# Performance work log

Measured on AMD Instinct MI355X. Metric: run time of the kernel, lower is better.

The kernel has to match this reference:

```python
import jax, jax.numpy as jnp
import numpy as np

D = 256
H = 4
HD = D // H


def rotate_half(x):
    xp = x.reshape(x.shape[:-1] + (-1, 2))
    x1, x2 = xp[..., 0], xp[..., 1]
    return jnp.stack((-x2, x1), axis=-1).reshape(x.shape)


def apply_rope(freqs, t):
    # freqs: [2, B, 1, N, HD]; t: [B, H, N, HD]
    return t * freqs[0] + rotate_half(t) * freqs[1]


def layernorm(x, g, b, eps=1e-5):
    m = jnp.mean(x, axis=-1, keepdims=True)
    v = jnp.var(x, axis=-1, keepdims=True)
    return (x - m) * jax.lax.rsqrt(v + eps) * g + b


def ffn(z, W1, b1, g, be, W2, b2):
    h = layernorm(z @ W1 + b1, g, be)
    h = jax.nn.gelu(h, approximate=False)
    return h @ W2 + b2


def heads_split(t):
    B, N, _ = t.shape
    return t.reshape(B, N, H, HD).transpose(0, 2, 1, 3)  # [B,H,N,HD]


def heads_merge(t):
    B, h, N, hd = t.shape
    return t.transpose(0, 2, 1, 3).reshape(B, N, h * hd)


def sdpa(q, k, v):
    s = q.shape[-1] ** (-0.5)
    sim = jnp.einsum('bhid,bhjd->bhij', q, k) * s
    attn = jax.nn.softmax(sim, axis=-1)
    return jnp.einsum('bhij,bhjd->bhid', attn, v)


def self_block(x, enc, Wqkv, bqkv, Wo, bo, W1, b1, g, be, W2, b2):
    B, N, _ = x.shape
    qkv = (x @ Wqkv + bqkv).reshape(B, N, H, HD, 3).transpose(0, 2, 1, 3, 4)
    q, k, v = qkv[..., 0], qkv[..., 1], qkv[..., 2]
    q = apply_rope(enc, q)
    k = apply_rope(enc, k)
    msg = heads_merge(sdpa(q, k, v)) @ Wo + bo
    return x + ffn(jnp.concatenate([x, msg], axis=-1), W1, b1, g, be, W2, b2)


def cross_block(x0, x1, Wqk, bqk, Wv, bv, Wo, bo, W1, b1, g, be, W2, b2):
    qk0 = heads_split(x0 @ Wqk + bqk)
    qk1 = heads_split(x1 @ Wqk + bqk)
    v0 = heads_split(x0 @ Wv + bv)
    v1 = heads_split(x1 @ Wv + bv)
    s = HD ** (-0.5)
    qk0 = qk0 * (s ** 0.5)
    qk1 = qk1 * (s ** 0.5)
    sim = jnp.einsum('bhid,bhjd->bhij', qk0, qk1)
    attn01 = jax.nn.softmax(sim, axis=-1)
    attn10 = jax.nn.softmax(sim.transpose(0, 1, 3, 2), axis=-1)
    m0 = jnp.einsum('bhij,bhjd->bhid', attn01, v1)
    m1 = jnp.einsum('bhij,bhjd->bhid', attn10, v0)
    m0 = heads_merge(m0) @ Wo + bo
    m1 = heads_merge(m1) @ Wo + bo
    x0 = x0 + ffn(jnp.concatenate([x0, m0], axis=-1), W1, b1, g, be, W2, b2)
    x1 = x1 + ffn(jnp.concatenate([x1, m1], axis=-1), W1, b1, g, be, W2, b2)
    return x0, x1


def setup_inputs() -> dict:
    key = jax.random.key(0)
    ks = jax.random.split(key, 24)
    B, N = 4, 2048
    desc0 = jax.random.normal(ks[0], (B, N, D), jnp.float32)
    desc1 = jax.random.normal(ks[1], (B, N, D), jnp.float32)
    encoding0 = jax.random.uniform(ks[2], (2, B, 1, N, HD), jnp.float32)
    encoding1 = jax.random.uniform(ks[3], (2, B, 1, N, HD), jnp.float32)

    def lin(k, fin, fout):
        k1, k2 = jax.random.split(k)
        W = jax.random.normal(k1, (fin, fout), jnp.float32) * (fin ** -0.5)
        b = jax.random.normal(k2, (fout,), jnp.float32) * 0.01
        return W, b

    Wqkv, bqkv = lin(ks[4], D, 3 * D)
    Wo_s, bo_s = lin(ks[5], D, D)
    W1_s, b1_s = lin(ks[6], 2 * D, 2 * D)
    g_s = jnp.ones((2 * D,), jnp.float32)
    be_s = jnp.zeros((2 * D,), jnp.float32)
    W2_s, b2_s = lin(ks[7], 2 * D, D)
    Wqk_c, bqk_c = lin(ks[8], D, D)
    Wv_c, bv_c = lin(ks[9], D, D)
    Wo_c, bo_c = lin(ks[10], D, D)
    W1_c, b1_c = lin(ks[11], 2 * D, 2 * D)
    g_c = jnp.ones((2 * D,), jnp.float32)
    be_c = jnp.zeros((2 * D,), jnp.float32)
    W2_c, b2_c = lin(ks[12], 2 * D, D)
    return dict(desc0=desc0, desc1=desc1, encoding0=encoding0, encoding1=encoding1,
                Wqkv=Wqkv, bqkv=bqkv, Wo_s=Wo_s, bo_s=bo_s,
                W1_s=W1_s, b1_s=b1_s, g_s=g_s, be_s=be_s, W2_s=W2_s, b2_s=b2_s,
                Wqk_c=Wqk_c, bqk_c=bqk_c, Wv_c=Wv_c, bv_c=bv_c, Wo_c=Wo_c, bo_c=bo_c,
                W1_c=W1_c, b1_c=b1_c, g_c=g_c, be_c=be_c, W2_c=W2_c, b2_c=b2_c)


def reference(desc0, desc1, encoding0, encoding1,
              Wqkv, bqkv, Wo_s, bo_s, W1_s, b1_s, g_s, be_s, W2_s, b2_s,
              Wqk_c, bqk_c, Wv_c, bv_c, Wo_c, bo_c, W1_c, b1_c, g_c, be_c, W2_c, b2_c):
    d0 = self_block(desc0, encoding0, Wqkv, bqkv, Wo_s, bo_s, W1_s, b1_s, g_s, be_s, W2_s, b2_s)
    d1 = self_block(desc1, encoding1, Wqkv, bqkv, Wo_s, bo_s, W1_s, b1_s, g_s, be_s, W2_s, b2_s)
    return cross_block(d0, d1, Wqk_c, bqk_c, Wv_c, bv_c, Wo_c, bo_c, W1_c, b1_c, g_c, be_c, W2_c, b2_c)
```

## Files before the change

kernel.cpp:

```cpp
#include <hip/hip_runtime.h>
#include <math.h>

#define BB 4
#define HH 4
#define NN 2048
#define DD 256
#define HDIM 64
#define NTOK 8192
#define NTOK2 16384

typedef __attribute__((ext_vector_type(8))) __bf16 bf16x8;
typedef __attribute__((ext_vector_type(8))) unsigned short ushort8;
typedef __attribute__((ext_vector_type(4))) float floatx4;
typedef __attribute__((ext_vector_type(4))) short short4v;

union U8 { ushort8 u; bf16x8 b; };
union U4 { unsigned int u[2]; unsigned long long l; short4v s; };

#define MFMA16(a, b, c) __builtin_amdgcn_mfma_f32_16x16x16bf16_1k(a, b, c, 0, 0, 0)

__device__ __forceinline__ unsigned short f2bf(float x) {
    unsigned int u = __float_as_uint(x);
    u += 0x7FFF + ((u >> 16) & 1);
    return (unsigned short)(u >> 16);
}
__device__ __forceinline__ float bf2f(unsigned short u) {
    return __uint_as_float(((unsigned int)u) << 16);
}
__device__ __forceinline__ unsigned int pkbf(float a, float b) {
    return ((__float_as_uint(a) + 0x8000u) >> 16) |
           ((__float_as_uint(b) + 0x8000u) & 0xFFFF0000u);
}
__device__ __forceinline__ unsigned int cvtpk(float a, float b) {
    unsigned int r;
    asm("v_cvt_pk_bf16_f32 %0, %1, %2" : "=v"(r) : "v"(a), "v"(b));
    return r;
}
__device__ __forceinline__ floatx4 fmax4(floatx4 a, floatx4 b) {
    floatx4 r;
    r[0] = fmaxf(a[0], b[0]); r[1] = fmaxf(a[1], b[1]);
    r[2] = fmaxf(a[2], b[2]); r[3] = fmaxf(a[3], b[3]);
    return r;
}

struct WTab {
    const float* w[7];
    unsigned short* o[7];
    int K[7];
    int N[7];
    int st[7];
    int t0[8];
};

__global__ __launch_bounds__(256) void wtrans(WTab tab)
{
    __shared__ float lds[32][33];
    const int t = threadIdx.x;
    int bid = blockIdx.x;
    int s = 0;
    while (bid >= tab.t0[s + 1]) s++;
    const int ti = bid - tab.t0[s];
    const int K = tab.K[s], N = tab.N[s], st = tab.st[s];
    const int tx = ti % (N / 32), ty = ti / (N / 32);
    const int k0 = ty * 32, n0 = tx * 32;
    const float* W = tab.w[s];
    unsigned short* Wt = tab.o[s];

    {
        int r = t >> 3, c = (t & 7) * 4;
        float4 a = *(const float4*)&W[(size_t)(k0 + r) * N + n0 + c];
        lds[r][c] = a.x; lds[r][c+1] = a.y; lds[r][c+2] = a.z; lds[r][c+3] = a.w;
    }
    __syncthreads();
    {
        int n = t >> 3, kq = (t & 7) * 4;
        ushort4 p;
        p.x = f2bf(lds[kq+0][n]); p.y = f2bf(lds[kq+1][n]);
        p.z = f2bf(lds[kq+2][n]); p.w = f2bf(lds[kq+3][n]);
        *(ushort4*)&Wt[(size_t)(n0 + n) * st + k0 + kq] = p;
    }
}

__global__ __launch_bounds__(256) void wfuse(
    const float* __restrict__ Wo_s, const float* __restrict__ W1_s,
    unsigned short* __restrict__ o_s,
    const float* __restrict__ Wo_c, const float* __restrict__ W1_c,
    unsigned short* __restrict__ o_c)
{
    __shared__ float wo[32][33];
    __shared__ float w1[32][68];
    const int t = threadIdx.x;
    const int bid = blockIdx.x;
    const int seg = bid >> 6, ti_ = bid & 63;
    const int i0 = (ti_ >> 3) * 32, n0 = (ti_ & 7) * 64;
    const float* Wo  = seg ? Wo_c : Wo_s;
    const float* W1b = (seg ? W1_c : W1_s) + 256 * 512;
    unsigned short* out = seg ? o_c : o_s;
    const int ti = t >> 3, tn = t & 7;

    float acc[8] = {};
    for (int jc = 0; jc < 256; jc += 32) {
        {
            int r = t >> 3, c = (t & 7) * 4;
            *(float4*)&wo[r][c] = *(const float4*)&Wo[(size_t)(i0 + r) * 256 + jc + c];
            int c8 = (t & 7) * 8;
            *(float4*)&w1[r][c8]     = *(const float4*)&W1b[(size_t)(jc + r) * 512 + n0 + c8];
            *(float4*)&w1[r][c8 + 4] = *(const float4*)&W1b[(size_t)(jc + r) * 512 + n0 + c8 + 4];
        }
        __syncthreads();
        #pragma unroll
        for (int j = 0; j < 32; j++) {
            float a = wo[ti][j];
            #pragma unroll
            for (int e = 0; e < 8; e++) acc[e] += a * w1[j][tn * 8 + e];
        }
        __syncthreads();
    }
    #pragma unroll
    for (int e = 0; e < 8; e++)
        out[(size_t)(n0 + tn * 8 + e) * 512 + 256 + i0 + ti] = f2bf(acc[e]);
}

__global__ __launch_bounds__(256) void bfuse(
    const float* bo_s, const float* W1_s, const float* b1_s, float* bs,
    const float* bo_c, const float* W1_c, const float* b1_c, float* bc)
{
    const int seg = blockIdx.x >> 1, half = blockIdx.x & 1;
    const int n = half * 256 + threadIdx.x;
    const float* bo  = seg ? bo_c : bo_s;
    const float* W1b = (seg ? W1_c : W1_s) + 256 * 512;
    const float* b1  = seg ? b1_c : b1_s;
    float* out       = seg ? bc : bs;
    float a = b1[n];
    for (int j = 0; j < 256; j++) a += bo[j] * W1b[(size_t)j * 512 + n];
    out[n] = a;
}

__global__ __launch_bounds__(256) void gemm_mfma(
    const unsigned short* __restrict__ A, int lda,
    const unsigned short* __restrict__ Wt, int K,
    const float* __restrict__ bias, const float* __restrict__ bias2, int mode,
    float* outF, unsigned short* outH0, unsigned short* outH1,
    unsigned short* outH2,
    int ldc, const float* R0, const float* R1)
{
    __shared__ __align__(16) unsigned short As[64 * 40];
    __shared__ __align__(16) unsigned short Bs[128 * 40];
    const int t = threadIdx.x;
    const int w = t >> 6, lane = t & 63, quad = lane >> 4, l15 = lane & 15;
    const int m0 = blockIdx.y * 64, n0 = blockIdx.x * 128;
    const int wn = w * 32;
    const int sar = t >> 2, sac = (t & 3) * 8;
    const int sbr = t >> 1, sbc = (t & 1) * 16;

    const unsigned short* Ap = A  + (size_t)(m0 + sar) * lda + sac;
    const unsigned short* Bp = Wt + (size_t)(n0 + sbr) * K   + sbc;

    ushort8 pa  = *(const ushort8*)(Ap);
    ushort8 pb0 = *(const ushort8*)(Bp);
    ushort8 pb1 = *(const ushort8*)(Bp + 8);

    floatx4 acc[4][2];
    #pragma unroll
    for (int i = 0; i < 4; i++)
        #pragma unroll
        for (int j = 0; j < 2; j++) acc[i][j] = (floatx4){0.f, 0.f, 0.f, 0.f};

    const int nk = K >> 5;
    for (int kk = 0; kk < nk; kk++) {
        *(ushort8*)&As[sar * 40 + sac]     = pa;
        *(ushort8*)&Bs[sbr * 40 + sbc]     = pb0;
        *(ushort8*)&Bs[sbr * 40 + sbc + 8] = pb1;
        __syncthreads();
        if (kk + 1 < nk) {
            int ko = (kk + 1) * 32;
            pa  = *(const ushort8*)(Ap + ko);
            pb0 = *(const ushort8*)(Bp + ko);
            pb1 = *(const ushort8*)(Bp + ko + 8);
        }
        U8 af[4], bf[2];
        #pragma unroll
        for (int i = 0; i < 4; i++)
            af[i].u = *(const ushort8*)&As[(i * 16 + l15) * 40 + quad * 8];
        #pragma unroll
        for (int j = 0; j < 2; j++)
            bf[j].u = *(const ushort8*)&Bs[(wn + j * 16 + l15) * 40 + quad * 8];
        #pragma unroll
        for (int i = 0; i < 4; i++)
            #pragma unroll
            for (int j = 0; j < 2; j++)
                acc[i][j] = __builtin_amdgcn_mfma_f32_16x16x32_bf16(af[i].b, bf[j].b, acc[i][j], 0, 0, 0);
        __syncthreads();
    }

    #pragma unroll
    for (int i = 0; i < 4; i++) {
        #pragma unroll
        for (int j = 0; j < 2; j++) {
            int col = n0 + wn + j * 16 + l15;
            float bv = (mode == 2 && col >= 256) ? bias2[col & 255] : bias[col];
            #pragma unroll
            for (int r = 0; r < 4; r++) {
                int grow = m0 + i * 16 + quad * 4 + r;
                float v = acc[i][j][r] + bv;
                if (mode == 1) {
                    outH0[(size_t)grow * ldc + col] = f2bf(v);
                } else if (mode == 2) {
                    int cc = col & 255;
                    int h = cc >> 6, d = cc & 63;
                    int ds = grow >> 13, b = (grow >> 11) & 3, n = grow & 2047;
                    int bh = ds * 16 + b * 4 + h;
                    if (col < 256)
                        outH0[((size_t)bh * NN + n) * HDIM + d] = f2bf(v);
                    else
                        outH1[((size_t)bh * HDIM + d) * NN + n] = f2bf(v);
                } else if (mode == 3) {
                    int sel = col % 3, cc = col / 3;
                    int h = cc >> 6, d = cc & 63;
                    int ds = grow >> 13, b = (grow >> 11) & 3, n = grow & 2047;
                    int bh = ds * 16 + b * 4 + h;
                    if (sel == 0)
                        outH0[((size_t)bh * NN + n) * HDIM + d] = f2bf(v);
                    else if (sel == 1)
                        outH1[((size_t)bh * NN + n) * HDIM + d] = f2bf(v);
                    else
                        outH2[((size_t)bh * HDIM + d) * NN + n] = f2bf(v);
                } else {
                    const float* R = (grow < NTOK) ? R0 : R1;
                    float vv = v + R[(size_t)(grow & 8191) * 256 + col];
                    outF[(size_t)grow * 256 + col] = vv;
                    if (outH0) outH0[(size_t)grow * 256 + col] = f2bf(vv);
                    if (outH1) outH1[(size_t)grow * 512 + col] = f2bf(vv);
                }
            }
        }
    }
}

__global__ __launch_bounds__(256) void rope_k(unsigned short* __restrict__ qb,
                                              unsigned short* __restrict__ kb,
                                              const float* __restrict__ enc0,
                                              const float* __restrict__ enc1)
{
    int i = blockIdx.x * 256 + threadIdx.x;
    int dp = (i & 31) * 2;
    int n  = (i >> 5) & (NN - 1);
    int h  = (i >> 16) & 3;
    int b  = (i >> 18) & 3;
    int ds = (i >> 20) & 1;
    int bf = (i >> 21) & 1;
    unsigned short* tq = (bf ? kb : qb) +
        (((size_t)(ds * 16 + b * 4 + h)) * NN + n) * HDIM + dp;
    const float* e0 = (ds ? enc1 : enc0) + ((size_t)b * NN + n) * HDIM + dp;
    const float* e1 = e0 + (size_t)BB * NN * HDIM;
    float x0 = bf2f(tq[0]), x1 = bf2f(tq[1]);
    float y0 = x0 * e0[0] - x1 * e1[0];
    float y1 = x1 * e0[1] + x0 * e1[1];
    tq[0] = f2bf(y0); tq[1] = f2bf(y1);
}

__global__ __launch_bounds__(256) void flash_attn(
    const unsigned short* __restrict__ Q, const unsigned short* __restrict__ K,
    const unsigned short* __restrict__ V, unsigned short* __restrict__ O,
    int ldo, int kvx, float qscale)
{
    __shared__ __align__(16) unsigned short Ks[2][64 * 72];
    __shared__ __align__(16) unsigned short Vt[2][64 * 72];

    const int t    = threadIdx.x;
    const int w    = t >> 6;
    const int lane = t & 63;
    const int quad = lane >> 4;
    const int l15  = lane & 15;
    const int bh   = blockIdx.y;
    const int kbh  = bh ^ kvx;
    const int q0   = blockIdx.x * 128;

    const unsigned short* Qb  = Q + (size_t)bh  * NN * HDIM;
    const unsigned short* Kb  = K + (size_t)kbh * NN * HDIM;
    const unsigned short* VTb = V + (size_t)kbh * NN * HDIM;

    const int srf = t >> 3, scf = (t & 7) * 8;

    bf16x8 qf0[2], qf1[2];
    #pragma unroll
    for (int i = 0; i < 2; i++) {
        const int qrow = q0 + w * 32 + i * 16 + l15;
        U8 r0, r1, x0, x1;
        r0.u = *(const ushort8*)&Qb[(size_t)qrow * HDIM + quad * 8];
        r1.u = *(const ushort8*)&Qb[(size_t)qrow * HDIM + 32 + quad * 8];
        #pragma unroll
        for (int j = 0; j < 8; j++) {
            x0.u[j] = f2bf(bf2f(r0.u[j]) * qscale);
            x1.u[j] = f2bf(bf2f(r1.u[j]) * qscale);
        }
        qf0[i] = x0.b; qf1[i] = x1.b;
    }

    floatx4 o[2][4];
    #pragma unroll
    for (int i = 0; i < 2; i++)
        #pragma unroll
        for (int c = 0; c < 4; c++) o[i][c] = (floatx4){0.f, 0.f, 0.f, 0.f};
    float m[2] = {-1e30f, -1e30f};
    float l[2] = {0.f, 0.f};

    ushort8 ka0 = *(const ushort8*)&Kb[(size_t)srf * HDIM + scf];
    ushort8 ka1 = *(const ushort8*)&Kb[(size_t)(srf + 32) * HDIM + scf];
    ushort8 va0 = *(const ushort8*)&VTb[(size_t)srf * NN + scf];
    ushort8 va1 = *(const ushort8*)&VTb[(size_t)(srf + 32) * NN + scf];
    *(ushort8*)&Ks[0][srf * 72 + scf]        = ka0;
    *(ushort8*)&Ks[0][(srf + 32) * 72 + scf] = ka1;
    *(ushort8*)&Vt[0][srf * 72 + scf]        = va0;
    *(ushort8*)&Vt[0][(srf + 32) * 72 + scf] = va1;
    __syncthreads();

    int cur = 0;
    for (int j0 = 0; j0 < NN; j0 += 64, cur ^= 1) {
        const int more = (j0 + 64 < NN);
        if (more) {
            const int jn = j0 + 64;
            ka0 = *(const ushort8*)&Kb[(size_t)(jn + srf) * HDIM + scf];
            ka1 = *(const ushort8*)&Kb[(size_t)(jn + srf + 32) * HDIM + scf];
            va0 = *(const ushort8*)&VTb[(size_t)srf * NN + jn + scf];
            va1 = *(const ushort8*)&VTb[(size_t)(srf + 32) * NN + jn + scf];
        }

        floatx4 s[2][4];
        __builtin_amdgcn_s_setprio(1);
        #pragma unroll
        for (int t4 = 0; t4 < 4; t4++) {
            U8 k0, k1;
            k0.u = *(const ushort8*)&Ks[cur][(t4 * 16 + l15) * 72 + quad * 8];
            k1.u = *(const ushort8*)&Ks[cur][(t4 * 16 + l15) * 72 + 32 + quad * 8];
            #pragma unroll
            for (int i = 0; i < 2; i++) {
                floatx4 z = (floatx4){0.f, 0.f, 0.f, 0.f};
                z = __builtin_amdgcn_mfma_f32_16x16x32_bf16(k0.b, qf0[i], z, 0, 0, 0);
                z = __builtin_amdgcn_mfma_f32_16x16x32_bf16(k1.b, qf1[i], z, 0, 0, 0);
                s[i][t4] = z;
            }
        }
        __builtin_amdgcn_s_setprio(0);

        short4v pf[2][4];
        #pragma unroll
        for (int i = 0; i < 2; i++) {
            floatx4 a = fmax4(fmax4(s[i][0], s[i][1]), fmax4(s[i][2], s[i][3]));
            float mx = fmaxf(fmaxf(a[0], a[1]), fmaxf(a[2], a[3]));
            mx = fmaxf(mx, __shfl_xor(mx, 16, 64));
            mx = fmaxf(mx, __shfl_xor(mx, 32, 64));
            if (!__all(mx <= m[i] + 8.f)) {
                float mn = fmaxf(m[i], mx);
                float al = exp2f(m[i] - mn);
                m[i] = mn;
                l[i] *= al;
                #pragma unroll
                for (int c = 0; c < 4; c++)
                    #pragma unroll
                    for (int r = 0; r < 4; r++) o[i][c][r] *= al;
            }
            float rs = 0.f;
            #pragma unroll
            for (int t4 = 0; t4 < 4; t4++)
                #pragma unroll
                for (int r = 0; r < 4; r++) {
                    float p = exp2f(s[i][t4][r] - m[i]);
                    s[i][t4][r] = p;
                    rs += p;
                }
            rs += __shfl_xor(rs, 16, 64);
            rs += __shfl_xor(rs, 32, 64);
            l[i] += rs;

            #pragma unroll
            for (int t4 = 0; t4 < 4; t4++) {
                U4 pk;
                pk.u[0] = cvtpk(s[i][t4][0], s[i][t4][1]);
                pk.u[1] = cvtpk(s[i][t4][2], s[i][t4][3]);
                pf[i][t4] = pk.s;
            }
        }

        __builtin_amdgcn_s_setprio(1);
        #pragma unroll
        for (int c = 0; c < 4; c++) {
            U4 vf[4];
            #pragma unroll
            for (int t4 = 0; t4 < 4; t4++)
                vf[t4].l = *(const unsigned long long*)
                    &Vt[cur][(c * 16 + l15) * 72 + t4 * 16 + quad * 4];
            #pragma unroll
            for (int i = 0; i < 2; i++)
                #pragma unroll
                for (int t4 = 0; t4 < 4; t4++)
                    o[i][c] = MFMA16(vf[t4].s, pf[i][t4], o[i][c]);
        }
        __builtin_amdgcn_s_setprio(0);

        if (more) {
            *(ushort8*)&Ks[cur ^ 1][srf * 72 + scf]        = ka0;
            *(ushort8*)&Ks[cur ^ 1][(srf + 32) * 72 + scf] = ka1;
            *(ushort8*)&Vt[cur ^ 1][srf * 72 + scf]        = va0;
            *(ushort8*)&Vt[cur ^ 1][(srf + 32) * 72 + scf] = va1;
            __syncthreads();
        }
    }

    const int ds = bh >> 4, b = (bh >> 2) & 3, h = bh & 3;
    #pragma unroll
    for (int i = 0; i < 2; i++) {
        const int q = q0 + w * 32 + i * 16 + l15;
        const size_t row = (size_t)ds * NTOK + b * NN + q;
        float inv = 1.f / l[i];
        #pragma unroll
        for (int c = 0; c < 4; c++) {
            U4 pk;
            pk.u[0] = cvtpk(o[i][c][0] * inv, o[i][c][1] * inv);
            pk.u[1] = cvtpk(o[i][c][2] * inv, o[i][c][3] * inv);
            *(unsigned long long*)&O[row * ldo + h * HDIM + c * 16 + quad * 4] = pk.l;
        }
    }
}

__global__ __launch_bounds__(256) void ln_gelu(
    unsigned short* __restrict__ hb, const float* __restrict__ g,
    const float* __restrict__ be)
{
    __shared__ float r1[4], r2[4];
    const int t = threadIdx.x;
    const size_t row = blockIdx.x;
    unsigned short* ip = hb + row * 512;
    float x0 = bf2f(ip[t]), x1 = bf2f(ip[t + 256]);
    float s = x0 + x1, ss = x0 * x0 + x1 * x1;
    #pragma unroll
    for (int o = 32; o > 0; o >>= 1) { s += __shfl_down(s, o); ss += __shfl_down(ss, o); }
    if ((t & 63) == 0) { r1[t >> 6] = s; r2[t >> 6] = ss; }
    __syncthreads();
    float S  = r1[0] + r1[1] + r1[2] + r1[3];
    float SS = r2[0] + r2[1] + r2[2] + r2[3];
    float mean = S * (1.f / 512.f);
    float var  = SS * (1.f / 512.f) - mean * mean;
    float inv  = rsqrtf(var + 1e-5f);
    float y0 = (x0 - mean) * inv * g[t]       + be[t];
    float y1 = (x1 - mean) * inv * g[t + 256] + be[t + 256];
    ip[t]       = f2bf(0.5f * y0 * (1.f + erff(y0 * 0.70710678f)));
    ip[t + 256] = f2bf(0.5f * y1 * (1.f + erff(y1 * 0.70710678f)));
}

__global__ __launch_bounds__(256) void copy_to_cat(
    const float* __restrict__ s0, const float* __restrict__ s1,
    unsigned short* __restrict__ cat)
{
    int i = blockIdx.x * 256 + threadIdx.x;
    int row = i >> 6, c4 = (i & 63) * 4;
    const float* s = (row < NTOK) ? s0 : s1;
    float4 a = *(const float4*)&s[(size_t)(row & 8191) * 256 + c4];
    ushort4 p = { f2bf(a.x), f2bf(a.y), f2bf(a.z), f2bf(a.w) };
    *(ushort4*)&cat[(size_t)row * 512 + c4] = p;
}

extern "C" void kernel_launch(void* const* d_in, const int* in_sizes, int n_in,
                              void* d_out, int out_size, void* d_ws, size_t ws_size,
                              hipStream_t stream)
{
    const float* desc0 = (const float*)d_in[0];
    const float* desc1 = (const float*)d_in[1];
    const float* enc0  = (const float*)d_in[2];
    const float* enc1  = (const float*)d_in[3];
    const float* Wqkv  = (const float*)d_in[4];  const float* bqkv  = (const float*)d_in[5];
    const float* Wo_s  = (const float*)d_in[6];  const float* bo_s  = (const float*)d_in[7];
    const float* W1_s  = (const float*)d_in[8];  const float* b1_s  = (const float*)d_in[9];
    const float* g_s   = (const float*)d_in[10]; const float* be_s  = (const float*)d_in[11];
    const float* W2_s  = (const float*)d_in[12]; const float* b2_s  = (const float*)d_in[13];
    const float* Wqk_c = (const float*)d_in[14]; const float* bqk_c = (const float*)d_in[15];
    const float* Wv_c  = (const float*)d_in[16]; const float* bv_c  = (const float*)d_in[17];
    const float* Wo_c  = (const float*)d_in[18]; const float* bo_c  = (const float*)d_in[19];
    const float* W1_c  = (const float*)d_in[20]; const float* b1_c  = (const float*)d_in[21];
    const float* g_c   = (const float*)d_in[22]; const float* be_c  = (const float*)d_in[23];
    const float* W2_c  = (const float*)d_in[24]; const float* b2_c  = (const float*)d_in[25];

    char* ws = (char*)d_ws;
    unsigned short* wt  = (unsigned short*)ws;
    unsigned short* qb  = (unsigned short*)(ws + 2490368);
    unsigned short* kb  = (unsigned short*)(ws + 10878976);
    unsigned short* vb  = (unsigned short*)(ws + 27656192);
    unsigned short* cat = (unsigned short*)(ws + 36044800);
    unsigned short* hb  = (unsigned short*)(ws + 52822016);
    unsigned short* dbf = (unsigned short*)(ws + 86376448);

    unsigned short* t_qkv  = wt;
    float*          bias_s = (float*)(wt + 196608);
    unsigned short* t_w1s  = wt + 262144;
    unsigned short* t_w2s  = wt + 524288;
    unsigned short* t_wqkc = wt + 655360;
    float*          bias_c = (float*)(wt + 786432);
    unsigned short* t_w1c  = wt + 851968;
    unsigned short* t_w2c  = wt + 1114112;

    float* outF = (float*)d_out;

    dim3 blk(256);

    WTab tab;
    tab.w[0] = Wqkv;  tab.o[0] = t_qkv;          tab.K[0] = 256; tab.N[0] = 768; tab.st[0] = 256;
    tab.w[1] = W1_s;  tab.o[1] = t_w1s;          tab.K[1] = 256; tab.N[1] = 512; tab.st[1] = 512;
    tab.w[2] = W2_s;  tab.o[2] = t_w2s;          tab.K[2] = 512; tab.N[2] = 256; tab.st[2] = 512;
    tab.w[3] = Wqk_c; tab.o[3] = t_wqkc;         tab.K[3] = 256; tab.N[3] = 256; tab.st[3] = 256;
    tab.w[4] = Wv_c;  tab.o[4] = t_wqkc + 65536; tab.K[4] = 256; tab.N[4] = 256; tab.st[4] = 256;
    tab.w[5] = W1_c;  tab.o[5] = t_w1c;          tab.K[5] = 256; tab.N[5] = 512; tab.st[5] = 512;
    tab.w[6] = W2_c;  tab.o[6] = t_w2c;          tab.K[6] = 512; tab.N[6] = 256; tab.st[6] = 512;
    int acc_t = 0;
    for (int s = 0; s < 7; s++) {
        tab.t0[s] = acc_t;
        acc_t += (tab.K[s] / 32) * (tab.N[s] / 32);
    }
    tab.t0[7] = acc_t;
    hipLaunchKernelGGL(wtrans, dim3(acc_t), blk, 0, stream, tab);
    hipLaunchKernelGGL(wfuse, dim3(128), blk, 0, stream,
                       Wo_s, W1_s, t_w1s, Wo_c, W1_c, t_w1c);
    hipLaunchKernelGGL(bfuse, dim3(4), blk, 0, stream,
                       bo_s, W1_s, b1_s, bias_s, bo_c, W1_c, b1_c, bias_c);

    auto gemm = [&](const unsigned short* A, int lda, const unsigned short* Wtp,
                    int K, const float* bias, const float* bias2, int Nc, int mode,
                    float* oF, unsigned short* oh0, unsigned short* oh1,
                    unsigned short* oh2, int ldc, const float* r0, const float* r1) {
        dim3 g(Nc / 128, NTOK2 / 64);
        hipLaunchKernelGGL(gemm_mfma, g, blk, 0, stream,
                           A, lda, Wtp, K, bias, bias2, mode,
                           oF, oh0, oh1, oh2, ldc, r0, r1);
    };

    const float QS = 0.125f * 1.44269504088896f;

    hipLaunchKernelGGL(copy_to_cat, dim3(4096), blk, 0, stream, desc0, desc1, cat);
    gemm(cat, 512, t_qkv, 256, bqkv, nullptr, 768, 3,
         nullptr, qb, kb, vb, 0, nullptr, nullptr);
    hipLaunchKernelGGL(rope_k, dim3(16384), blk, 0, stream, qb, kb, enc0, enc1);
    hipLaunchKernelGGL(flash_attn, dim3(NN / 128, 32), blk, 0, stream,
                       qb, kb, vb, cat + 256, 512, 0, QS);
    gemm(cat, 512, t_w1s, 512, bias_s, nullptr, 512, 1,
         nullptr, hb, nullptr, nullptr, 512, nullptr, nullptr);
    hipLaunchKernelGGL(ln_gelu, dim3(NTOK2), blk, 0, stream, hb, g_s, be_s);
    gemm(hb, 512, t_w2s, 512, b2_s, nullptr, 256, 4,
         outF, dbf, cat, nullptr, 256, desc0, desc1);

    gemm(dbf, 256, t_wqkc, 256, bqk_c, bv_c, 512, 2,
         nullptr, qb, vb, nullptr, 0, nullptr, nullptr);
    hipLaunchKernelGGL(flash_attn, dim3(NN / 128, 32), blk, 0, stream,
                       qb, qb, vb, cat + 256, 512, 16, QS);
    gemm(cat, 512, t_w1c, 512, bias_c, nullptr, 512, 1,
         nullptr, hb, nullptr, nullptr, 512, nullptr, nullptr);
    hipLaunchKernelGGL(ln_gelu, dim3(NTOK2), blk, 0, stream, hb, g_c, be_c);
    gemm(hb, 512, t_w2c, 512, b2_c, nullptr, 256, 4,
         outF, nullptr, nullptr, nullptr, 256, outF, outF + (size_t)NTOK * 256);
}
```

Baseline: 486.6 us.

## Use direct global-to-LDS loads and 128-row GEMM tiles; make layernorm one row per wave

The GEMM now loads A and B tiles straight into LDS with global_load_lds instead of staging them through registers. It also drops the padded LDS stride and adds a 128x128 tile variant with a 2x2 wave layout for the wider (N=512/768) GEMMs. This raises data reuse per block and removes register staging, but it also removes the register prefetch overlap and may add LDS bank conflicts from the unpadded layout. The LayerNorm+GELU kernel is rewritten to handle one row per wavefront with 8-wide vector loads and shuffle-only reductions, which removes the LDS reduction and block barrier.

```diff
diff --git a/kernel.cpp b/kernel.cpp
--- a/kernel.cpp
+++ b/kernel.cpp
@@ -27,10 +27,6 @@
 __device__ __forceinline__ float bf2f(unsigned short u) {
     return __uint_as_float(((unsigned int)u) << 16);
 }
-__device__ __forceinline__ unsigned int pkbf(float a, float b) {
-    return ((__float_as_uint(a) + 0x8000u) >> 16) |
-           ((__float_as_uint(b) + 0x8000u) & 0xFFFF0000u);
-}
 __device__ __forceinline__ unsigned int cvtpk(float a, float b) {
     unsigned int r;
     asm("v_cvt_pk_bf16_f32 %0, %1, %2" : "=v"(r) : "v"(a), "v"(b));
@@ -41,6 +37,11 @@
     r[0] = fmaxf(a[0], b[0]); r[1] = fmaxf(a[1], b[1]);
     r[2] = fmaxf(a[2], b[2]); r[3] = fmaxf(a[3], b[3]);
     return r;
+}
+__device__ __forceinline__ void gload16(const unsigned short* g, unsigned short* l) {
+    __builtin_amdgcn_global_load_lds(
+        (const __attribute__((address_space(1))) unsigned int*)g,
+        (__attribute__((address_space(3))) unsigned int*)l, 16, 0, 0);
 }
 
 struct WTab {
@@ -136,6 +137,7 @@
     out[n] = a;
 }
 
+template<int BM>
 __global__ __launch_bounds__(256) void gemm_mfma(
     const unsigned short* __restrict__ A, int lda,
     const unsigned short* __restrict__ Wt, int K,
@@ -144,51 +146,54 @@
     unsigned short* outH2,
     int ldc, const float* R0, const float* R1)
 {
-    __shared__ __align__(16) unsigned short As[64 * 40];
-    __shared__ __align__(16) unsigned short Bs[128 * 40];
+    constexpr int NJ  = (BM == 128) ? 4 : 2;
+    constexpr int NCA = BM / 64;
+    __shared__ __align__(16) unsigned short As[BM * 32];
+    __shared__ __align__(16) unsigned short Bs[128 * 32];
     const int t = threadIdx.x;
     const int w = t >> 6, lane = t & 63, quad = lane >> 4, l15 = lane & 15;
-    const int m0 = blockIdx.y * 64, n0 = blockIdx.x * 128;
-    const int wn = w * 32;
-    const int sar = t >> 2, sac = (t & 3) * 8;
-    const int sbr = t >> 1, sbc = (t & 1) * 16;
-
-    const unsigned short* Ap = A  + (size_t)(m0 + sar) * lda + sac;
-    const unsigned short* Bp = Wt + (size_t)(n0 + sbr) * K   + sbc;
-
-    ushort8 pa  = *(const ushort8*)(Ap);
-    ushort8 pb0 = *(const ushort8*)(Bp);
-    ushort8 pb1 = *(const ushort8*)(Bp + 8);
-
-    floatx4 acc[4][2];
+    const int m0 = blockIdx.y * BM, n0 = blockIdx.x * 128;
+    const int wrow = (BM == 128) ? (w >> 1) * 64 : 0;
+    const int wcol = (BM == 128) ? (w & 1) * 64 : w * 32;
+
+    const int lr = lane >> 2, lc4 = (lane & 3) * 8;
+    const unsigned short* Ag[NCA];
+    #pragma unroll
+    for (int q = 0; q < NCA; q++)
+        Ag[q] = A + (size_t)(m0 + (w * NCA + q) * 16 + lr) * lda + lc4;
+    const unsigned short* Bg[2];
+    #pragma unroll
+    for (int q = 0; q < 2; q++)
+        Bg[q] = Wt + (size_t)(n0 + (w * 2 + q) * 16 + lr) * K + lc4;
+
+    floatx4 acc[4][NJ];
     #pragma unroll
     for (int i = 0; i < 4; i++)
         #pragma unroll
-        for (int j = 0; j < 2; j++) acc[i][j] = (floatx4){0.f, 0.f, 0.f, 0.f};
+        for (int j = 0; j < NJ; j++) acc[i][j] = (floatx4){0.f, 0.f, 0.f, 0.f};
 
     const int nk = K >> 5;
     for (int kk = 0; kk < nk; kk++) {
-        *(ushort8*)&As[sar * 40 + sac]     = pa;
-        *(ushort8*)&Bs[sbr * 40 + sbc]     = pb0;
-        *(ushort8*)&Bs[sbr * 40 + sbc + 8] = pb1;
+        const int ko = kk * 32;
+        #pragma unroll
+        for (int q = 0; q < NCA; q++)
+            gload16(Ag[q] + ko, &As[(w * NCA + q) * 512]);
+        #pragma unroll
+        for (int q = 0; q < 2; q++)
+            gload16(Bg[q] + ko, &Bs[(w * 2 + q) * 512]);
         __syncthreads();
-        if (kk + 1 < nk) {
-            int ko = (kk + 1) * 32;
-            pa  = *(const ushort8*)(Ap + ko);
-            pb0 = *(const ushort8*)(Bp + ko);
-            pb1 = *(const ushort8*)(Bp + ko + 8);
-        }
-        U8 af[4], bf[2];
+
+        U8 af[4], bf[NJ];
         #pragma unroll
         for (int i = 0; i < 4; i++)
-            af[i].u = *(const ushort8*)&As[(i * 16 + l15) * 40 + quad * 8];
-        #pragma unroll
-        for (int j = 0; j < 2; j++)
-            bf[j].u = *(const ushort8*)&Bs[(wn + j * 16 + l15) * 40 + quad * 8];
+            af[i].u = *(const ushort8*)&As[(wrow + i * 16 + l15) * 32 + quad * 8];
+        #pragma unroll
+        for (int j = 0; j < NJ; j++)
+            bf[j].u = *(const ushort8*)&Bs[(wcol + j * 16 + l15) * 32 + quad * 8];
         #pragma unroll
         for (int i = 0; i < 4; i++)
             #pragma unroll
-            for (int j = 0; j < 2; j++)
+            for (int j = 0; j < NJ; j++)
                 acc[i][j] = __builtin_amdgcn_mfma_f32_16x16x32_bf16(af[i].b, bf[j].b, acc[i][j], 0, 0, 0);
         __syncthreads();
     }
@@ -196,12 +201,12 @@
     #pragma unroll
     for (int i = 0; i < 4; i++) {
         #pragma unroll
-        for (int j = 0; j < 2; j++) {
-            int col = n0 + wn + j * 16 + l15;
+        for (int j = 0; j < NJ; j++) {
+            int col = n0 + wcol + j * 16 + l15;
             float bv = (mode == 2 && col >= 256) ? bias2[col & 255] : bias[col];
             #pragma unroll
             for (int r = 0; r < 4; r++) {
-                int grow = m0 + i * 16 + quad * 4 + r;
+                int grow = m0 + wrow + i * 16 + quad * 4 + r;
                 float v = acc[i][j][r] + bv;
                 if (mode == 1) {
                     outH0[(size_t)grow * ldc + col] = f2bf(v);
@@ -427,25 +432,39 @@
     unsigned short* __restrict__ hb, const float* __restrict__ g,
     const float* __restrict__ be)
 {
-    __shared__ float r1[4], r2[4];
-    const int t = threadIdx.x;
-    const size_t row = blockIdx.x;
-    unsigned short* ip = hb + row * 512;
-    float x0 = bf2f(ip[t]), x1 = bf2f(ip[t + 256]);
-    float s = x0 + x1, ss = x0 * x0 + x1 * x1;
-    #pragma unroll
-    for (int o = 32; o > 0; o >>= 1) { s += __shfl_down(s, o); ss += __shfl_down(ss, o); }
-    if ((t & 63) == 0) { r1[t >> 6] = s; r2[t >> 6] = ss; }
-    __syncthreads();
-    float S  = r1[0] + r1[1] + r1[2] + r1[3];
-    float SS = r2[0] + r2[1] + r2[2] + r2[3];
-    float mean = S * (1.f / 512.f);
-    float var  = SS * (1.f / 512.f) - mean * mean;
+    const int lane = threadIdx.x & 63;
+    const int wv   = threadIdx.x >> 6;
+    const size_t row = (size_t)blockIdx.x * 4 + wv;
+    unsigned short* ip = hb + row * 512 + lane * 8;
+    U8 v; v.u = *(const ushort8*)ip;
+    float x[8];
+    float s = 0.f, ss = 0.f;
+    #pragma unroll
+    for (int j = 0; j < 8; j++) {
+        x[j] = bf2f(v.u[j]);
+        s += x[j];
+        ss += x[j] * x[j];
+    }
+    #pragma unroll
+    for (int o = 32; o > 0; o >>= 1) {
+        s  += __shfl_xor(s, o, 64);
+        ss += __shfl_xor(ss, o, 64);
+    }
+    float mean = s * (1.f / 512.f);
+    float var  = ss * (1.f / 512.f) - mean * mean;
     float inv  = rsqrtf(var + 1e-5f);
-    float y0 = (x0 - mean) * inv * g[t]       + be[t];
-    float y1 = (x1 - mean) * inv * g[t + 256] + be[t + 256];
-    ip[t]       = f2bf(0.5f * y0 * (1.f + erff(y0 * 0.70710678f)));
-    ip[t + 256] = f2bf(0.5f * y1 * (1.f + erff(y1 * 0.70710678f)));
+    float4 g0 = *(const float4*)&g[lane * 8];
+    float4 g1 = *(const float4*)&g[lane * 8 + 4];
+    float4 b0 = *(const float4*)&be[lane * 8];
+    float4 b1 = *(const float4*)&be[lane * 8 + 4];
+    float gg[8] = {g0.x, g0.y, g0.z, g0.w, g1.x, g1.y, g1.z, g1.w};
+    float bb[8] = {b0.x, b0.y, b0.z, b0.w, b1.x, b1.y, b1.z, b1.w};
+    #pragma unroll
+    for (int j = 0; j < 8; j++) {
+        float y = (x[j] - mean) * inv * gg[j] + bb[j];
+        v.u[j] = f2bf(0.5f * y * (1.f + erff(y * 0.70710678f)));
+    }
+    *(ushort8*)ip = v.u;
 }
 
 __global__ __launch_bounds__(256) void copy_to_cat(
@@ -526,10 +545,17 @@
                     int K, const float* bias, const float* bias2, int Nc, int mode,
                     float* oF, unsigned short* oh0, unsigned short* oh1,
                     unsigned short* oh2, int ldc, const float* r0, const float* r1) {
-        dim3 g(Nc / 128, NTOK2 / 64);
-        hipLaunchKernelGGL(gemm_mfma, g, blk, 0, stream,
-                           A, lda, Wtp, K, bias, bias2, mode,
-                           oF, oh0, oh1, oh2, ldc, r0, r1);
+        if (Nc == 256) {
+            dim3 g2(Nc / 128, NTOK2 / 64);
+            hipLaunchKernelGGL((gemm_mfma<64>), g2, blk, 0, stream,
+                               A, lda, Wtp, K, bias, bias2, mode,
+                               oF, oh0, oh1, oh2, ldc, r0, r1);
+        } else {
+            dim3 g2(Nc / 128, NTOK2 / 128);
+            hipLaunchKernelGGL((gemm_mfma<128>), g2, blk, 0, stream,
+                               A, lda, Wtp, K, bias, bias2, mode,
+                               oF, oh0, oh1, oh2, ldc, r0, r1);
+        }
     };
 
     const float QS = 0.125f * 1.44269504088896f;
@@ -542,7 +568,7 @@
                        qb, kb, vb, cat + 256, 512, 0, QS);
     gemm(cat, 512, t_w1s, 512, bias_s, nullptr, 512, 1,
          nullptr, hb, nullptr, nullptr, 512, nullptr, nullptr);
-    hipLaunchKernelGGL(ln_gelu, dim3(NTOK2), blk, 0, stream, hb, g_s, be_s);
+    hipLaunchKernelGGL(ln_gelu, dim3(NTOK2 / 4), blk, 0, stream, hb, g_s, be_s);
     gemm(hb, 512, t_w2s, 512, b2_s, nullptr, 256, 4,
          outF, dbf, cat, nullptr, 256, desc0, desc1);
 
@@ -552,7 +578,7 @@
                        qb, qb, vb, cat + 256, 512, 16, QS);
     gemm(cat, 512, t_w1c, 512, bias_c, nullptr, 512, 1,
          nullptr, hb, nullptr, nullptr, 512, nullptr, nullptr);
-    hipLaunchKernelGGL(ln_gelu, dim3(NTOK2), blk, 0, stream, hb, g_c, be_c);
+    hipLaunchKernelGGL(ln_gelu, dim3(NTOK2 / 4), blk, 0, stream, hb, g_c, be_c);
     gemm(hb, 512, t_w2c, 512, b2_c, nullptr, 256, 4,
          outF, nullptr, nullptr, nullptr, 256, outF, outF + (size_t)NTOK * 256);
 }
```

Result: slower. 511.9 us (+5.2%).
